# Kernel optimization log

Hardware: AMD Instinct MI355X
Metric: run time of the kernel (lower is better)

Reference implementation:

```python
import jax, jax.numpy as jnp
import numpy as np

H, C = 4, 64            # heads, channels per head (graph_hidden_channels)
GHC = H * C             # concat width = 256
FIN = 32                # num_node_features
NHID = 256
NOUT = 256
NEG_SLOPE = 0.2         # PyG GATConv default negative_slope


def gat_conv(x, src, dst, n, W, a_src, a_dst, bias):
    # x: [N, Fin], W: [Fin, H*C], a_src/a_dst: [H, C], bias: [H*C]
    h = (x @ W).reshape(n, H, C)                       # [N,H,C]
    s = (h * a_src).sum(-1)                            # [N,H] src logits
    d = (h * a_dst).sum(-1)                            # [N,H] dst logits
    e = jax.nn.leaky_relu(s[src] + d[dst], NEG_SLOPE)  # [E,H]
    m = jax.ops.segment_max(e, dst, num_segments=n)    # segment softmax (stable)
    ex = jnp.exp(e - m[dst])
    denom = jax.ops.segment_sum(ex, dst, num_segments=n)
    alpha = ex / jnp.maximum(denom[dst], 1e-16)        # [E,H]
    msg = h[src] * alpha[:, :, None]                   # [E,H,C]
    out = jax.ops.segment_sum(msg, dst, num_segments=n)
    return out.reshape(n, GHC) + bias


def setup_inputs() -> dict:
    key = jax.random.key(0)
    ks = jax.random.split(key, 32)
    N, E, G = 50000, 800000, 256
    inp = {
        'x': jax.random.normal(ks[0], (N, FIN), dtype=jnp.float32),
        'edge_index': jax.random.randint(ks[1], (2, E), 0, N, dtype=jnp.int32),
        'batch': jnp.sort(jax.random.randint(ks[2], (N,), 0, G, dtype=jnp.int32)),
        'num_graphs': G,
    }
    def p(k, shape):
        return jax.random.normal(k, shape, dtype=jnp.float32) * 0.05
    # three GATConv layers + head linears
    ins = [FIN, C, C]
    i = 3
    for l, fin in enumerate(ins, start=1):
        inp[f'W{l}'] = p(ks[i], (fin, GHC)); i += 1
        inp[f'a{l}s'] = p(ks[i], (H, C)); i += 1
        inp[f'a{l}d'] = p(ks[i], (H, C)); i += 1
        inp[f'b{l}'] = p(ks[i], (GHC,)); i += 1
        inp[f'hl{l}_w'] = p(ks[i], (GHC, C)); i += 1
        inp[f'hl{l}_b'] = p(ks[i], (C,)); i += 1
    inp['mh1_w'] = p(ks[i], (C, NHID)); i += 1
    inp['mh1_b'] = p(ks[i], (NHID,)); i += 1
    inp['mh2_w'] = p(ks[i], (NHID, NOUT)); i += 1
    inp['mh2_b'] = p(ks[i], (NOUT,))
    return inp


def reference(x, edge_index, batch, num_graphs,
              W1, a1s, a1d, b1, hl1_w, hl1_b,
              W2, a2s, a2d, b2, hl2_w, hl2_b,
              W3, a3s, a3d, b3, hl3_w, hl3_b,
              mh1_w, mh1_b, mh2_w, mh2_b):
    n = x.shape[0]
    loops = jnp.arange(n, dtype=edge_index.dtype)  # PyG add_self_loops=True
    src = jnp.concatenate([edge_index[0], loops])
    dst = jnp.concatenate([edge_index[1], loops])

    h = gat_conv(x, src, dst, n, W1, a1s, a1d, b1)
    h = jax.nn.relu(h @ hl1_w + hl1_b)
    h = gat_conv(h, src, dst, n, W2, a2s, a2d, b2)
    h = jax.nn.relu(h @ hl2_w + hl2_b)
    h = gat_conv(h, src, dst, n, W3, a3s, a3d, b3)
    h = h @ hl3_w + hl3_b                      # no relu before pooling (as in source)

    sums = jax.ops.segment_sum(h, batch, num_segments=num_graphs)
    cnt = jax.ops.segment_sum(jnp.ones((n,), h.dtype), batch, num_segments=num_graphs)
    g = sums / jnp.maximum(cnt, 1.0)[:, None]  # global_mean_pool

    g = jax.nn.relu(g @ mh1_w + mh1_b)
    return g @ mh2_w + mh2_b
```

## Files before the change

kernel.cpp:

```cpp
#include <hip/hip_runtime.h>
#include <hip/hip_bf16.h>
#include <hip/hip_fp16.h>
#include <math.h>

#define HD 4
#define CH 64
#define GHC 256
#define NEG 0.2f
#define CHUNK 4096
#define BCAP 16384

#define WAVE_SYNC() do { __builtin_amdgcn_wave_barrier(); \
                         asm volatile("s_waitcnt lgkmcnt(0)" ::: "memory"); } while (0)

typedef _Float16 f16x8 __attribute__((ext_vector_type(8)));
typedef float f32x4 __attribute__((ext_vector_type(4)));

__device__ __forceinline__ float wsum32(float v){
  #pragma unroll
  for (int o = 16; o > 0; o >>= 1) v += __shfl_xor(v, o);
  return v;
}

__global__ __launch_bounds__(256)
void front_kernel(const int* __restrict__ ei, int E, int N, int cb_blocks,
                  int* __restrict__ bres, unsigned* __restrict__ pairs,
                  const float* __restrict__ W1, const float* __restrict__ a1s,
                  const float* __restrict__ a1d, const float* __restrict__ b1,
                  const float* __restrict__ h1w, const float* __restrict__ h1b,
                  const float* __restrict__ W2, const float* __restrict__ a2s,
                  const float* __restrict__ a2d, const float* __restrict__ b2,
                  const float* __restrict__ h2w, const float* __restrict__ h2b,
                  const float* __restrict__ W3, const float* __restrict__ a3s,
                  const float* __restrict__ a3d, const float* __restrict__ b3,
                  const float* __restrict__ h3w, const float* __restrict__ h3b,
                  __half* __restrict__ Wpk1, float* __restrict__ Psd1, float* __restrict__ cb1,
                  __half* __restrict__ Wpk2, __half* __restrict__ Ppk2, float* __restrict__ cb2,
                  float* __restrict__ Wcp3, __half* __restrict__ Ppk3, float* __restrict__ cb3,
                  const int* __restrict__ batch, int G, int* __restrict__ bnd)
{
  __shared__ unsigned staged[CHUNK];
  __shared__ unsigned short bkt[CHUNK];
  __shared__ int cnts[256], loff[256], gpos[256];
  const int t = threadIdx.x;

  if (blockIdx.x < cb_blocks){
    const int tot = E + N;
    const int cbase = blockIdx.x * CHUNK;
    if (cbase >= tot) return;

    cnts[t] = 0;
    __syncthreads();

    unsigned myp[CHUNK / 256];
    int myb[CHUNK / 256], myr[CHUNK / 256];
    #pragma unroll
    for (int j = 0; j < CHUNK / 256; j++){
      int i = cbase + t + j * 256;
      myb[j] = -1;
      if (i < tot){
        int src, dst;
        if (i < E){ src = ei[i]; dst = ei[E + i]; }
        else { src = dst = i - E; }
        myb[j] = dst >> 8;
        myp[j] = (unsigned)src | ((unsigned)dst << 16);
        myr[j] = atomicAdd(&cnts[myb[j]], 1);
      }
    }
    __syncthreads();

    int v = cnts[t];
    loff[t] = v;
    __syncthreads();
    for (int o = 1; o < 256; o <<= 1){
      int tv = (t >= o) ? loff[t - o] : 0;
      __syncthreads();
      loff[t] += tv;
      __syncthreads();
    }
    int excl = loff[t] - v;
    __syncthreads();
    loff[t] = excl;
    __syncthreads();

    #pragma unroll
    for (int j = 0; j < CHUNK / 256; j++){
      if (myb[j] >= 0){
        int slot = loff[myb[j]] + myr[j];
        staged[slot] = myp[j];
        bkt[slot] = (unsigned short)myb[j];
      }
    }
    if (v > 0) gpos[t] = atomicAdd(&bres[t], v);
    __syncthreads();

    int total = min(CHUNK, tot - cbase);
    for (int i = t; i < total; i += 256){
      int b = bkt[i];
      int addr = b * BCAP + gpos[b] + (i - loff[b]);
      pairs[addr] = staged[i];
    }
    return;
  }

  const int blk = blockIdx.x - cb_blocks;
  if (blk >= 163){
    int g = (blk - 163) * 256 + t;
    if (g > G) return;
    if (g == G){ bnd[G] = N; return; }
    int lo = 0, hi = N;
    while (lo < hi){ int mid = (lo + hi) >> 1; if (batch[mid] < g) lo = mid + 1; else hi = mid; }
    bnd[g] = lo;
    return;
  }
  const float *W, *as, *ad, *bl, *hlw, *hlb;
  float *cb;
  int FIN, b, layer;
  if (blk < 33){
    W = W1; as = a1s; ad = a1d; bl = b1; hlw = h1w; hlb = h1b;
    cb = cb1; FIN = 32; b = blk; layer = 1;
  } else if (blk < 98){
    W = W2; as = a2s; ad = a2d; bl = b2; hlw = h2w; hlb = h2b;
    cb = cb2; FIN = 64; b = blk - 33; layer = 2;
  } else {
    W = W3; as = a3s; ad = a3d; bl = b3; hlw = h3w; hlb = h3b;
    cb = cb3; FIN = 64; b = blk - 98; layer = 3;
  }
  if (b < FIN){
    const int c = t >> 2, h = t & 3;
    const float* wrow = W + b * GHC + h * 64;
    float acc = 0.f;
    #pragma unroll 8
    for (int j = 0; j < 64; j++)
      acc += wrow[j] * hlw[(h * 64 + j) * CH + c];
    const int k = h * FIN + b;
    if (layer == 3){
      Wcp3[k * CH + c] = acc;
    } else {
      int ks = k >> 5, nt = c >> 4;
      int lane = (((k & 31) >> 3) << 4) | (c & 15);
      int idx = ((ks * 4 + nt) * 64 + lane) * 8 + (k & 7);
      __half* Wpk = (layer == 1) ? Wpk1 : Wpk2;
      Wpk[idx] = __float2half(acc);
    }
    if (t < 8){
      const int hh = t & 3;
      const float* a = (t < 4) ? as : ad;
      const float* wr2 = W + b * GHC + hh * 64;
      float p = 0.f;
      #pragma unroll 8
      for (int j = 0; j < 64; j++) p += wr2[j] * a[hh * 64 + j];
      if (layer == 1){
        Psd1[b * 8 + t] = p;
      } else {
        int kk = b;
        int ks = kk >> 5;
        int lane = (((kk & 31) >> 3) << 4) | t;
        int idx = (ks * 64 + lane) * 8 + (kk & 7);
        __half* Ppk = (layer == 2) ? Ppk2 : Ppk3;
        Ppk[idx] = __float2half(p);
      }
    }
  } else if (t < CH){
    float acc = hlb[t];
    for (int j = 0; j < GHC; j++) acc += bl[j] * hlw[j * CH + t];
    cb[t] = acc;
  }
}

__global__ __launch_bounds__(256)
void mid_kernel(const unsigned* __restrict__ pairs, const int* __restrict__ bres,
                int N, int Etot, int nbuck,
                int* __restrict__ offs, unsigned short* __restrict__ csr,
                const float* __restrict__ x, const float* __restrict__ Psd,
                float* __restrict__ s_log, float* __restrict__ d_log,
                __half* __restrict__ xh0)
{
  __shared__ int dcnt[256], doff[256], bscan[256];
  const int t = threadIdx.x;

  if (blockIdx.x < nbuck){
    const int b = blockIdx.x;
    int bv = bres[t];
    bscan[t] = bv;
    __syncthreads();
    for (int o = 1; o < 256; o <<= 1){
      int tv = (t >= o) ? bscan[t - o] : 0;
      __syncthreads();
      bscan[t] += tv;
      __syncthreads();
    }
    const int beg = bscan[b] - bres[b];
    const int cnt = bres[b];
    const unsigned* pb = pairs + (size_t)b * BCAP;
    dcnt[t] = 0;
    __syncthreads();
    for (int i = t; i < cnt; i += 256)
      atomicAdd(&dcnt[(pb[i] >> 16) & 255], 1);
    __syncthreads();
    int v = dcnt[t];
    doff[t] = v;
    __syncthreads();
    for (int o = 1; o < 256; o <<= 1){
      int tv = (t >= o) ? doff[t - o] : 0;
      __syncthreads();
      doff[t] += tv;
      __syncthreads();
    }
    int excl = doff[t] - v;
    __syncthreads();
    doff[t] = excl;
    __syncthreads();
    int node = (b << 8) + t;
    if (node < N) offs[node] = beg + doff[t];
    if (b == 0 && t == 0) offs[N] = Etot;
    dcnt[t] = 0;
    __syncthreads();
    for (int i = t; i < cnt; i += 256){
      unsigned pr = pb[i];
      int l = (pr >> 16) & 255;
      int pos = beg + doff[l] + atomicAdd(&dcnt[l], 1);
      csr[pos] = (unsigned short)(pr & 0xFFFF);
    }
    return;
  }

  int idx = (blockIdx.x - nbuck) * 256 + t;
  int node = idx >> 3, q = idx & 7;
  if (node >= N) return;
  const float* xr = x + (size_t)node * 32;
  float v = 0.f;
  #pragma unroll 8
  for (int k = 0; k < 32; k++) v += xr[k] * Psd[k * 8 + q];
  if (q < 4){
    s_log[node * 4 + q] = v;
    __half2 h0 = __floats2half2_rn(xr[q*8+0], xr[q*8+1]);
    __half2 h1 = __floats2half2_rn(xr[q*8+2], xr[q*8+3]);
    __half2 h2 = __floats2half2_rn(xr[q*8+4], xr[q*8+5]);
    __half2 h3 = __floats2half2_rn(xr[q*8+6], xr[q*8+7]);
    uint4 u;
    u.x = *reinterpret_cast<const unsigned*>(&h0);
    u.y = *reinterpret_cast<const unsigned*>(&h1);
    u.z = *reinterpret_cast<const unsigned*>(&h2);
    u.w = *reinterpret_cast<const unsigned*>(&h3);
    *reinterpret_cast<uint4*>(xh0 + (size_t)node * 32 + q * 8) = u;
  } else {
    d_log[node * 4 + (q - 4)] = v;
  }
}

template<int F, int ZW>
__global__ __launch_bounds__(512)
void gat_layer_fused(const __half* __restrict__ xin, const float* __restrict__ s_in,
                     const float* __restrict__ d_in_, const int* __restrict__ off,
                     const unsigned short* __restrict__ csr,
                     const __half* __restrict__ Wpk, const float* __restrict__ cb,
                     const __half* __restrict__ Ppk,
                     __half* __restrict__ xo, float* __restrict__ s_out,
                     float* __restrict__ d_out_, int N)
{
  constexpr int ZP = ZW + 8;
  __shared__ float4 qa[8][2][32];
  __shared__ int    qs[8][2][32];
  __shared__ __half z_lds[16][ZP];
  __shared__ float  outs[16][68];
  __shared__ float  cbs[64];
  const int tid  = threadIdx.x;
  const int wv   = tid >> 6;
  const int lane = tid & 63;
  const int half = lane >> 5;
  const int l32  = lane & 31;
  const int n0 = blockIdx.x * 16;
  const int n = n0 + wv * 2 + half;
  const bool valid = n < N;
  if (tid < 64) cbs[tid] = cb[tid];

  int beg = 0, deg = 0;
  if (valid){ beg = off[n]; deg = off[n + 1] - beg; }

  float d4[4] = {0.f, 0.f, 0.f, 0.f};
  if (valid){
    float4 d4v = reinterpret_cast<const float4*>(d_in_)[n];
    d4[0] = d4v.x; d4[1] = d4v.y; d4[2] = d4v.z; d4[3] = d4v.w;
  }

  float den[4], ex[4];
  int s = 0;
  {
    const bool act = valid && (l32 < deg);
    if (act){
      s = csr[beg + l32];
      float4 sl = reinterpret_cast<const float4*>(s_in)[s];
      float t[4] = {sl.x, sl.y, sl.z, sl.w};
      #pragma unroll
      for (int i = 0; i < 4; i++){
        float u = t[i] + d4[i]; u = (u >= 0.f) ? u : NEG * u;
        ex[i] = __expf(u);
      }
    } else {
      #pragma unroll
      for (int i = 0; i < 4; i++) ex[i] = 0.f;
    }
    #pragma unroll
    for (int i = 0; i < 4; i++) den[i] = wsum32(ex[i]);
  }
  for (int base = 32; base < deg; base += 32){
    const int k = base + l32;
    float e2[4] = {0.f, 0.f, 0.f, 0.f};
    if (k < deg){
      int s2 = csr[beg + k];
      float4 sl = reinterpret_cast<const float4*>(s_in)[s2];
      float t[4] = {sl.x, sl.y, sl.z, sl.w};
      #pragma unroll
      for (int i = 0; i < 4; i++){
        float u = t[i] + d4[i]; u = (u >= 0.f) ? u : NEG * u;
        e2[i] = __expf(u);
      }
    }
    #pragma unroll
    for (int i = 0; i < 4; i++) den[i] += wsum32(e2[i]);
  }

  float dninv[4];
  #pragma unroll
  for (int i = 0; i < 4; i++) dninv[i] = 1.f / fmaxf(den[i], 1e-16f);

  float a0[4] = {0.f,0.f,0.f,0.f};
  float a1[4] = {0.f,0.f,0.f,0.f};
  const float4* qap = qa[wv][half];
  const int*    qsp = qs[wv][half];

  auto accum = [&](int cnt){
    int cntR = (cnt + 3) & ~3;
    if (F == 64){
      const __half* xb = xin + 2 * l32;
      for (int e0 = 0; e0 < cntR; e0 += 4){
        float4 al[4]; int sv[4]; unsigned uv[4];
        #pragma unroll
        for (int j = 0; j < 4; j++){ al[j] = qap[e0 + j]; sv[j] = qsp[e0 + j]; }
        #pragma unroll
        for (int j = 0; j < 4; j++)
          uv[j] = *reinterpret_cast<const unsigned*>(xb + sv[j] * 64);
        #pragma unroll
        for (int j = 0; j < 4; j++){
          float2 f = __half22float2(*reinterpret_cast<const __half2*>(&uv[j]));
          a0[0] += al[j].x * f.x; a1[0] += al[j].x * f.y;
          a0[1] += al[j].y * f.x; a1[1] += al[j].y * f.y;
          a0[2] += al[j].z * f.x; a1[2] += al[j].z * f.y;
          a0[3] += al[j].w * f.x; a1[3] += al[j].w * f.y;
        }
      }
    } else {
      const __half* xb = xin + l32;
      for (int e0 = 0; e0 < cntR; e0 += 4){
        float4 al[4]; int sv[4]; __half hv[4];
        #pragma unroll
        for (int j = 0; j < 4; j++){ al[j] = qap[e0 + j]; sv[j] = qsp[e0 + j]; }
        #pragma unroll
        for (int j = 0; j < 4; j++)
          hv[j] = xb[sv[j] * 32];
        #pragma unroll
        for (int j = 0; j < 4; j++){
          float xv = __half2float(hv[j]);
          a0[0] += al[j].x * xv;
          a0[1] += al[j].y * xv;
          a0[2] += al[j].z * xv;
          a0[3] += al[j].w * xv;
        }
      }
    }
  };

  if (deg <= 32){
    qa[wv][half][l32] = make_float4(ex[0] * dninv[0], ex[1] * dninv[1],
                                    ex[2] * dninv[2], ex[3] * dninv[3]);
    qs[wv][half][l32] = s;
    WAVE_SYNC();
    accum(deg);
  } else {
    for (int base = 0; base < deg; base += 32){
      const int k = base + l32;
      int s2 = 0; float al[4] = {0.f, 0.f, 0.f, 0.f};
      if (k < deg){
        s2 = csr[beg + k];
        float4 sl = reinterpret_cast<const float4*>(s_in)[s2];
        float t[4] = {sl.x, sl.y, sl.z, sl.w};
        #pragma unroll
        for (int i = 0; i < 4; i++){
          float u = t[i] + d4[i]; u = (u >= 0.f) ? u : NEG * u;
          al[i] = __expf(u) * dninv[i];
        }
      }
      qa[wv][half][l32] = make_float4(al[0], al[1], al[2], al[3]);
      qs[wv][half][l32] = s2;
      WAVE_SYNC();
      accum(min(32, deg - base));
      WAVE_SYNC();
    }
  }

  {
    const int r = wv * 2 + half;
    if (F == 64){
      #pragma unroll
      for (int h = 0; h < 4; h++){
        __half2 hv = __floats2half2_rn(a0[h], a1[h]);
        *reinterpret_cast<unsigned*>(&z_lds[r][h * 64 + 2 * l32]) =
            *reinterpret_cast<const unsigned*>(&hv);
      }
    } else {
      #pragma unroll
      for (int h = 0; h < 4; h++)
        z_lds[r][h * 32 + l32] = __float2half(a0[h]);
    }
  }
  __syncthreads();

  const int row = lane & 15, kg = lane >> 4;
  if (wv < 4){
    const int nt = wv;
    f32x4 acc = {0.f,0.f,0.f,0.f};
    const f16x8* wp = reinterpret_cast<const f16x8*>(Wpk) + lane;
    #pragma unroll
    for (int ks = 0; ks < ZW / 32; ks++){
      f16x8 af = *reinterpret_cast<const f16x8*>(&z_lds[row][kg * 8 + ks * 32]);
      acc = __builtin_amdgcn_mfma_f32_16x16x32_f16(af, wp[(ks*4+nt)*64], acc, 0,0,0);
    }
    #pragma unroll
    for (int r = 0; r < 4; r++){
      int rr = kg * 4 + r;
      outs[rr][nt * 16 + row] = fmaxf(acc[r] + cbs[nt * 16 + row], 0.f);
    }
  }
  __syncthreads();

  if (tid < 256){
    int nn = tid >> 4, part = tid & 15;
    int node = n0 + nn;
    if (node < N){
      const float* o = &outs[nn][part * 4];
      __half2 h0 = __floats2half2_rn(o[0], o[1]);
      __half2 h1 = __floats2half2_rn(o[2], o[3]);
      uint2 u;
      u.x = *reinterpret_cast<const unsigned*>(&h0);
      u.y = *reinterpret_cast<const unsigned*>(&h1);
      *reinterpret_cast<uint2*>(xo + (size_t)node * 64 + part * 4) = u;
    }
  }

  if (wv == 4){
    f32x4 lacc = {0.f,0.f,0.f,0.f};
    const f16x8* pp = reinterpret_cast<const f16x8*>(Ppk) + lane;
    #pragma unroll
    for (int ks = 0; ks < 2; ks++){
      f16x8 af;
      #pragma unroll
      for (int j = 0; j < 8; j++) af[j] = (_Float16)outs[row][ks * 32 + kg * 8 + j];
      lacc = __builtin_amdgcn_mfma_f32_16x16x32_f16(af, pp[ks * 64], lacc, 0,0,0);
    }
    if (row < 8){
      float* dst = (row < 4) ? s_out : d_out_;
      int q = row & 3;
      #pragma unroll
      for (int r = 0; r < 4; r++){
        int node = n0 + kg * 4 + r;
        if (node < N) dst[node * 4 + q] = lacc[r];
      }
    }
  }
}

template<int F>
__global__ __launch_bounds__(256)
void gat_aggregate_z(const __half* __restrict__ xin, const float* __restrict__ s_log,
                     const float* __restrict__ d_log, const int* __restrict__ off,
                     const unsigned short* __restrict__ csr, __half* __restrict__ z, int N)
{
  __shared__ float4 qa[4][2][32];
  __shared__ int    qs[4][2][32];
  const int wv   = threadIdx.x >> 6;
  const int lane = threadIdx.x & 63;
  const int half = lane >> 5;
  const int l32  = lane & 31;
  const int n = blockIdx.x * 8 + wv * 2 + half;
  const bool valid = n < N;

  int beg = 0, deg = 0;
  if (valid){ beg = off[n]; deg = off[n + 1] - beg; }

  float d4[4] = {0.f, 0.f, 0.f, 0.f};
  if (valid){
    float4 d4v = reinterpret_cast<const float4*>(d_log)[n];
    d4[0] = d4v.x; d4[1] = d4v.y; d4[2] = d4v.z; d4[3] = d4v.w;
  }

  float den[4], ex[4];
  int s = 0;
  {
    const bool act = valid && (l32 < deg);
    if (act){
      s = csr[beg + l32];
      float4 sl = reinterpret_cast<const float4*>(s_log)[s];
      float t[4] = {sl.x, sl.y, sl.z, sl.w};
      #pragma unroll
      for (int i = 0; i < 4; i++){
        float u = t[i] + d4[i]; u = (u >= 0.f) ? u : NEG * u;
        ex[i] = __expf(u);
      }
    } else {
      #pragma unroll
      for (int i = 0; i < 4; i++) ex[i] = 0.f;
    }
    #pragma unroll
    for (int i = 0; i < 4; i++) den[i] = wsum32(ex[i]);
  }
  for (int base = 32; base < deg; base += 32){
    const int k = base + l32;
    float e2[4] = {0.f, 0.f, 0.f, 0.f};
    if (k < deg){
      int s2 = csr[beg + k];
      float4 sl = reinterpret_cast<const float4*>(s_log)[s2];
      float t[4] = {sl.x, sl.y, sl.z, sl.w};
      #pragma unroll
      for (int i = 0; i < 4; i++){
        float u = t[i] + d4[i]; u = (u >= 0.f) ? u : NEG * u;
        e2[i] = __expf(u);
      }
    }
    #pragma unroll
    for (int i = 0; i < 4; i++) den[i] += wsum32(e2[i]);
  }

  float dninv[4];
  #pragma unroll
  for (int i = 0; i < 4; i++) dninv[i] = 1.f / fmaxf(den[i], 1e-16f);

  float a0[4] = {0.f,0.f,0.f,0.f};
  float a1[4] = {0.f,0.f,0.f,0.f};
  const float4* qap = qa[wv][half];
  const int*    qsp = qs[wv][half];

  auto accum = [&](int cnt){
    int cntR = (cnt + 3) & ~3;
    const __half* xb = xin + 2 * l32;
    for (int e0 = 0; e0 < cntR; e0 += 4){
      float4 al[4]; int sv[4]; unsigned uv[4];
      #pragma unroll
      for (int j = 0; j < 4; j++){ al[j] = qap[e0 + j]; sv[j] = qsp[e0 + j]; }
      #pragma unroll
      for (int j = 0; j < 4; j++)
        uv[j] = *reinterpret_cast<const unsigned*>(xb + sv[j] * 64);
      #pragma unroll
      for (int j = 0; j < 4; j++){
        float2 f = __half22float2(*reinterpret_cast<const __half2*>(&uv[j]));
        a0[0] += al[j].x * f.x; a1[0] += al[j].x * f.y;
        a0[1] += al[j].y * f.x; a1[1] += al[j].y * f.y;
        a0[2] += al[j].z * f.x; a1[2] += al[j].z * f.y;
        a0[3] += al[j].w * f.x; a1[3] += al[j].w * f.y;
      }
    }
  };

  if (deg <= 32){
    qa[wv][half][l32] = make_float4(ex[0] * dninv[0], ex[1] * dninv[1],
                                    ex[2] * dninv[2], ex[3] * dninv[3]);
    qs[wv][half][l32] = s;
    WAVE_SYNC();
    accum(deg);
  } else {
    for (int base = 0; base < deg; base += 32){
      const int k = base + l32;
      int s2 = 0; float al[4] = {0.f, 0.f, 0.f, 0.f};
      if (k < deg){
        s2 = csr[beg + k];
        float4 sl = reinterpret_cast<const float4*>(s_log)[s2];
        float t[4] = {sl.x, sl.y, sl.z, sl.w};
        #pragma unroll
        for (int i = 0; i < 4; i++){
          float u = t[i] + d4[i]; u = (u >= 0.f) ? u : NEG * u;
          al[i] = __expf(u) * dninv[i];
        }
      }
      qa[wv][half][l32] = make_float4(al[0], al[1], al[2], al[3]);
      qs[wv][half][l32] = s2;
      WAVE_SYNC();
      accum(min(32, deg - base));
      WAVE_SYNC();
    }
  }

  if (valid){
    const size_t zb = (size_t)n * 256 + 2 * l32;
    #pragma unroll
    for (int h = 0; h < 4; h++){
      __half2 hv = __floats2half2_rn(a0[h], a1[h]);
      *reinterpret_cast<unsigned*>(z + zb + h * 64) =
          *reinterpret_cast<const unsigned*>(&hv);
    }
  }
}

__global__ __launch_bounds__(256)
void pool_partial(const __half* __restrict__ z3, const int* __restrict__ bnd,
                  float* __restrict__ psum)
{
  const int blk = blockIdx.x, tid = threadIdx.x;
  const int g = blk >> 2, part = blk & 3;
  const int s = bnd[g], e = bnd[g + 1];
  const int cp = tid & 127, rp = tid >> 7;
  float ax = 0.f, ay = 0.f;
  for (int n = s + part + 4 * rp; n < e; n += 8){
    __half2 hv = *reinterpret_cast<const __half2*>(z3 + (size_t)n * 256 + 2 * cp);
    float2 f = __half22float2(hv);
    ax += f.x; ay += f.y;
  }
  __shared__ float shx[2][128], shy[2][128];
  shx[rp][cp] = ax; shy[rp][cp] = ay;
  __syncthreads();
  if (tid < 128){
    psum[(size_t)blk * 256 + 2 * tid]     = shx[0][tid] + shx[1][tid];
    psum[(size_t)blk * 256 + 2 * tid + 1] = shy[0][tid] + shy[1][tid];
  }
}

__global__ __launch_bounds__(256)
void head_mlp(const float* __restrict__ psum, const int* __restrict__ bnd,
              const float* __restrict__ Wcp3, const float* __restrict__ cb3,
              const float* __restrict__ m1w, const float* __restrict__ m1b,
              const float* __restrict__ m2w, const float* __restrict__ m2b,
              float* __restrict__ out)
{
  const int g = blockIdx.x, tid = threadIdx.x;
  const float cnt = (float)max(bnd[g + 1] - bnd[g], 1);
  __shared__ float zbar[256];
  const float* pb = psum + (size_t)g * 1024;
  zbar[tid] = (pb[tid] + pb[256 + tid] + pb[512 + tid] + pb[768 + tid]) / cnt;
  __syncthreads();
  const int c = tid & 63, part = tid >> 6;
  float tp = 0.f;
  #pragma unroll 8
  for (int k = part * 64; k < part * 64 + 64; k++) tp += zbar[k] * Wcp3[k * 64 + c];
  __shared__ float tsh[4][64];
  tsh[part][c] = tp;
  __syncthreads();
  __shared__ float tvec[64];
  if (tid < 64)
    tvec[tid] = tsh[0][tid] + tsh[1][tid] + tsh[2][tid] + tsh[3][tid] + cb3[tid];
  __syncthreads();
  float a = m1b[tid];
  #pragma unroll 8
  for (int cc = 0; cc < 64; cc++) a += tvec[cc] * m1w[cc * 256 + tid];
  __shared__ float g1row[256];
  g1row[tid] = fmaxf(a, 0.f);
  __syncthreads();
  float o = m2b[tid];
  #pragma unroll 8
  for (int k = 0; k < 256; k++) o += g1row[k] * m2w[k * 256 + tid];
  out[g * 256 + tid] = o;
}

extern "C" void kernel_launch(void* const* d_in, const int* in_sizes, int n_in,
                              void* d_out, int out_size, void* d_ws, size_t ws_size,
                              hipStream_t stream)
{
  const float* x     = (const float*)d_in[0];
  const int*   ei    = (const int*)d_in[1];
  const int*   batch = (const int*)d_in[2];
  const float* W1  = (const float*)d_in[4];
  const float* a1s = (const float*)d_in[5];
  const float* a1d = (const float*)d_in[6];
  const float* b1  = (const float*)d_in[7];
  const float* h1w = (const float*)d_in[8];
  const float* h1b = (const float*)d_in[9];
  const float* W2  = (const float*)d_in[10];
  const float* a2s = (const float*)d_in[11];
  const float* a2d = (const float*)d_in[12];
  const float* b2  = (const float*)d_in[13];
  const float* h2w = (const float*)d_in[14];
  const float* h2b = (const float*)d_in[15];
  const float* W3  = (const float*)d_in[16];
  const float* a3s = (const float*)d_in[17];
  const float* a3d = (const float*)d_in[18];
  const float* b3  = (const float*)d_in[19];
  const float* h3w = (const float*)d_in[20];
  const float* h3b = (const float*)d_in[21];
  const float* m1w = (const float*)d_in[22];
  const float* m1b = (const float*)d_in[23];
  const float* m2w = (const float*)d_in[24];
  const float* m2b = (const float*)d_in[25];

  const int N = in_sizes[0] / 32;
  const int E = in_sizes[1] / 2;
  const int G = out_size / 256;
  const int Etot = E + N;
  const int nbuck = (N + 255) >> 8;

  char* p = (char*)d_ws;
  auto alloc = [&](size_t bytes) -> void* {
    void* r = (void*)p;
    p += ((bytes + 255) / 256) * 256;
    return r;
  };
  __half* zbuf   = (__half*)alloc((size_t)N * GHC * 2);
  __half* xh0    = (__half*)alloc((size_t)N * 32 * 2);
  __half* xh1    = (__half*)alloc((size_t)N * CH * 2);
  __half* xh2    = (__half*)alloc((size_t)N * CH * 2);
  float* s_logA  = (float*)alloc((size_t)N * HD * 4);
  float* d_logA  = (float*)alloc((size_t)N * HD * 4);
  float* s_logB  = (float*)alloc((size_t)N * HD * 4);
  float* d_logB  = (float*)alloc((size_t)N * HD * 4);
  int*   offs    = (int*)alloc((size_t)(N + 1) * 4);
  unsigned short* csr = (unsigned short*)alloc((size_t)Etot * 2);
  unsigned* pairs = (unsigned*)alloc((size_t)nbuck * BCAP * 4);
  int*    bres   = (int*)alloc(256 * 4);
  __half* Ppk2   = (__half*)alloc(1024 * 2);
  __half* Ppk3   = (__half*)alloc(1024 * 2);
  int*   bnd     = (int*)alloc((size_t)(G + 1) * 4);
  float* psum    = (float*)alloc((size_t)G * 4 * 256 * 4);
  float* Wcp3    = (float*)alloc(256 * 64 * 4);
  float* Psd1    = (float*)alloc(32 * 8 * 4);
  float* cb1     = (float*)alloc(64 * 4);
  float* cb2     = (float*)alloc(64 * 4);
  float* cb3     = (float*)alloc(64 * 4);
  __half* Wpk1   = (__half*)alloc(128 * 64 * 2);
  __half* Wpk2   = (__half*)alloc(256 * 64 * 2);

  hipMemsetAsync(bres, 0, 5120, stream);

  const int cb_blocks = (Etot + CHUNK - 1) / CHUNK;
  const int fuse_blocks = 163 + (G + 256) / 256;
  front_kernel<<<cb_blocks + fuse_blocks, 256, 0, stream>>>(
      ei, E, N, cb_blocks, bres, pairs,
      W1, a1s, a1d, b1, h1w, h1b,
      W2, a2s, a2d, b2, h2w, h2b,
      W3, a3s, a3d, b3, h3w, h3b,
      Wpk1, Psd1, cb1, Wpk2, Ppk2, cb2, Wcp3, Ppk3, cb3,
      batch, G, bnd);

  const int lg_blocks = ((size_t)N * 8 + 255) / 256;
  mid_kernel<<<nbuck + lg_blocks, 256, 0, stream>>>(
      pairs, bres, N, Etot, nbuck, offs, csr,
      x, Psd1, s_logA, d_logA, xh0);

  const int fgrid = (N + 15) / 16;
  gat_layer_fused<32, 128><<<fgrid, 512, 0, stream>>>(xh0, s_logA, d_logA, offs, csr,
                                                      Wpk1, cb1, Ppk2, xh1, s_logB, d_logB, N);
  gat_layer_fused<64, 256><<<fgrid, 512, 0, stream>>>(xh1, s_logB, d_logB, offs, csr,
                                                      Wpk2, cb2, Ppk3, xh2, s_logA, d_logA, N);

  const int ab = (N + 7) / 8;
  gat_aggregate_z<64><<<ab, 256, 0, stream>>>(xh2, s_logA, d_logA, offs, csr, zbuf, N);

  pool_partial<<<G * 4, 256, 0, stream>>>(zbuf, bnd, psum);
  head_mlp<<<G, 256, 0, stream>>>(psum, bnd, Wcp3, cb3, m1w, m1b, m2w, m2b, (float*)d_out);
}
```

Baseline: 150.1 us.

## Fuse layer-3 head linear into fused GAT kernel and pool 64-wide outputs

Replaces the separate layer-3 aggregate kernel, which wrote a 256-wide fp16 z buffer per node, with the fused GAT layer template (no ReLU, no logits), which applies the folded W3·hl3 projection via MFMA and writes 64-wide node outputs. Pooling then reads 64 channels instead of 256, and the head MLP no longer applies the Wcp3 projection after pooling. This cuts the large z write and read traffic. The cost is a per-node projection in place of a per-graph one, and fp16 rounding now falls at a different point.

```diff
diff --git a/kernel.cpp b/kernel.cpp
--- a/kernel.cpp
+++ b/kernel.cpp
@@ -36,7 +36,7 @@
                   const float* __restrict__ h3w, const float* __restrict__ h3b,
                   __half* __restrict__ Wpk1, float* __restrict__ Psd1, float* __restrict__ cb1,
                   __half* __restrict__ Wpk2, __half* __restrict__ Ppk2, float* __restrict__ cb2,
-                  float* __restrict__ Wcp3, __half* __restrict__ Ppk3, float* __restrict__ cb3,
+                  __half* __restrict__ Wpk3, __half* __restrict__ Ppk3, float* __restrict__ cb3,
                   const int* __restrict__ batch, int G, int* __restrict__ bnd)
 {
   __shared__ unsigned staged[CHUNK];
@@ -134,13 +134,11 @@
     for (int j = 0; j < 64; j++)
       acc += wrow[j] * hlw[(h * 64 + j) * CH + c];
     const int k = h * FIN + b;
-    if (layer == 3){
-      Wcp3[k * CH + c] = acc;
-    } else {
+    {
       int ks = k >> 5, nt = c >> 4;
       int lane = (((k & 31) >> 3) << 4) | (c & 15);
       int idx = ((ks * 4 + nt) * 64 + lane) * 8 + (k & 7);
-      __half* Wpk = (layer == 1) ? Wpk1 : Wpk2;
+      __half* Wpk = (layer == 1) ? Wpk1 : ((layer == 2) ? Wpk2 : Wpk3);
       Wpk[idx] = __float2half(acc);
     }
     if (t < 8){
@@ -249,7 +247,7 @@
   }
 }
 
-template<int F, int ZW>
+template<int F, int ZW, bool RELU, bool LOGITS>
 __global__ __launch_bounds__(512)
 void gat_layer_fused(const __half* __restrict__ xin, const float* __restrict__ s_in,
                      const float* __restrict__ d_in_, const int* __restrict__ off,
@@ -429,7 +427,9 @@
     #pragma unroll
     for (int r = 0; r < 4; r++){
       int rr = kg * 4 + r;
-      outs[rr][nt * 16 + row] = fmaxf(acc[r] + cbs[nt * 16 + row], 0.f);
+      float v = acc[r] + cbs[nt * 16 + row];
+      if (RELU) v = fmaxf(v, 0.f);
+      outs[rr][nt * 16 + row] = v;
     }
   }
   __syncthreads();
@@ -448,7 +448,7 @@
     }
   }
 
-  if (wv == 4){
+  if (LOGITS && wv == 4){
     f32x4 lacc = {0.f,0.f,0.f,0.f};
     const f16x8* pp = reinterpret_cast<const f16x8*>(Ppk) + lane;
     #pragma unroll
@@ -470,182 +470,44 @@
   }
 }
 
-template<int F>
 __global__ __launch_bounds__(256)
-void gat_aggregate_z(const __half* __restrict__ xin, const float* __restrict__ s_log,
-                     const float* __restrict__ d_log, const int* __restrict__ off,
-                     const unsigned short* __restrict__ csr, __half* __restrict__ z, int N)
-{
-  __shared__ float4 qa[4][2][32];
-  __shared__ int    qs[4][2][32];
-  const int wv   = threadIdx.x >> 6;
-  const int lane = threadIdx.x & 63;
-  const int half = lane >> 5;
-  const int l32  = lane & 31;
-  const int n = blockIdx.x * 8 + wv * 2 + half;
-  const bool valid = n < N;
-
-  int beg = 0, deg = 0;
-  if (valid){ beg = off[n]; deg = off[n + 1] - beg; }
-
-  float d4[4] = {0.f, 0.f, 0.f, 0.f};
-  if (valid){
-    float4 d4v = reinterpret_cast<const float4*>(d_log)[n];
-    d4[0] = d4v.x; d4[1] = d4v.y; d4[2] = d4v.z; d4[3] = d4v.w;
-  }
-
-  float den[4], ex[4];
-  int s = 0;
-  {
-    const bool act = valid && (l32 < deg);
-    if (act){
-      s = csr[beg + l32];
-      float4 sl = reinterpret_cast<const float4*>(s_log)[s];
-      float t[4] = {sl.x, sl.y, sl.z, sl.w};
-      #pragma unroll
-      for (int i = 0; i < 4; i++){
-        float u = t[i] + d4[i]; u = (u >= 0.f) ? u : NEG * u;
-        ex[i] = __expf(u);
-      }
-    } else {
-      #pragma unroll
-      for (int i = 0; i < 4; i++) ex[i] = 0.f;
-    }
-    #pragma unroll
-    for (int i = 0; i < 4; i++) den[i] = wsum32(ex[i]);
-  }
-  for (int base = 32; base < deg; base += 32){
-    const int k = base + l32;
-    float e2[4] = {0.f, 0.f, 0.f, 0.f};
-    if (k < deg){
-      int s2 = csr[beg + k];
-      float4 sl = reinterpret_cast<const float4*>(s_log)[s2];
-      float t[4] = {sl.x, sl.y, sl.z, sl.w};
-      #pragma unroll
-      for (int i = 0; i < 4; i++){
-        float u = t[i] + d4[i]; u = (u >= 0.f) ? u : NEG * u;
-        e2[i] = __expf(u);
-      }
-    }
-    #pragma unroll
-    for (int i = 0; i < 4; i++) den[i] += wsum32(e2[i]);
-  }
-
-  float dninv[4];
-  #pragma unroll
-  for (int i = 0; i < 4; i++) dninv[i] = 1.f / fmaxf(den[i], 1e-16f);
-
-  float a0[4] = {0.f,0.f,0.f,0.f};
-  float a1[4] = {0.f,0.f,0.f,0.f};
-  const float4* qap = qa[wv][half];
-  const int*    qsp = qs[wv][half];
-
-  auto accum = [&](int cnt){
-    int cntR = (cnt + 3) & ~3;
-    const __half* xb = xin + 2 * l32;
-    for (int e0 = 0; e0 < cntR; e0 += 4){
-      float4 al[4]; int sv[4]; unsigned uv[4];
-      #pragma unroll
-      for (int j = 0; j < 4; j++){ al[j] = qap[e0 + j]; sv[j] = qsp[e0 + j]; }
-      #pragma unroll
-      for (int j = 0; j < 4; j++)
-        uv[j] = *reinterpret_cast<const unsigned*>(xb + sv[j] * 64);
-      #pragma unroll
-      for (int j = 0; j < 4; j++){
-        float2 f = __half22float2(*reinterpret_cast<const __half2*>(&uv[j]));
-        a0[0] += al[j].x * f.x; a1[0] += al[j].x * f.y;
-        a0[1] += al[j].y * f.x; a1[1] += al[j].y * f.y;
-        a0[2] += al[j].z * f.x; a1[2] += al[j].z * f.y;
-        a0[3] += al[j].w * f.x; a1[3] += al[j].w * f.y;
-      }
-    }
-  };
-
-  if (deg <= 32){
-    qa[wv][half][l32] = make_float4(ex[0] * dninv[0], ex[1] * dninv[1],
-                                    ex[2] * dninv[2], ex[3] * dninv[3]);
-    qs[wv][half][l32] = s;
-    WAVE_SYNC();
-    accum(deg);
-  } else {
-    for (int base = 0; base < deg; base += 32){
-      const int k = base + l32;
-      int s2 = 0; float al[4] = {0.f, 0.f, 0.f, 0.f};
-      if (k < deg){
-        s2 = csr[beg + k];
-        float4 sl = reinterpret_cast<const float4*>(s_log)[s2];
-        float t[4] = {sl.x, sl.y, sl.z, sl.w};
-        #pragma unroll
-        for (int i = 0; i < 4; i++){
-          float u = t[i] + d4[i]; u = (u >= 0.f) ? u : NEG * u;
-          al[i] = __expf(u) * dninv[i];
-        }
-      }
-      qa[wv][half][l32] = make_float4(al[0], al[1], al[2], al[3]);
-      qs[wv][half][l32] = s2;
-      WAVE_SYNC();
-      accum(min(32, deg - base));
-      WAVE_SYNC();
-    }
-  }
-
-  if (valid){
-    const size_t zb = (size_t)n * 256 + 2 * l32;
-    #pragma unroll
-    for (int h = 0; h < 4; h++){
-      __half2 hv = __floats2half2_rn(a0[h], a1[h]);
-      *reinterpret_cast<unsigned*>(z + zb + h * 64) =
-          *reinterpret_cast<const unsigned*>(&hv);
-    }
-  }
-}
-
-__global__ __launch_bounds__(256)
-void pool_partial(const __half* __restrict__ z3, const int* __restrict__ bnd,
+void pool_partial(const __half* __restrict__ x3, const int* __restrict__ bnd,
                   float* __restrict__ psum)
 {
   const int blk = blockIdx.x, tid = threadIdx.x;
   const int g = blk >> 2, part = blk & 3;
   const int s = bnd[g], e = bnd[g + 1];
-  const int cp = tid & 127, rp = tid >> 7;
+  const int cp = tid & 31, rp = tid >> 5;
   float ax = 0.f, ay = 0.f;
-  for (int n = s + part + 4 * rp; n < e; n += 8){
-    __half2 hv = *reinterpret_cast<const __half2*>(z3 + (size_t)n * 256 + 2 * cp);
+  for (int n = s + part + 4 * rp; n < e; n += 32){
+    __half2 hv = *reinterpret_cast<const __half2*>(x3 + (size_t)n * 64 + 2 * cp);
     float2 f = __half22float2(hv);
     ax += f.x; ay += f.y;
   }
-  __shared__ float shx[2][128], shy[2][128];
+  __shared__ float shx[8][32], shy[8][32];
   shx[rp][cp] = ax; shy[rp][cp] = ay;
   __syncthreads();
-  if (tid < 128){
-    psum[(size_t)blk * 256 + 2 * tid]     = shx[0][tid] + shx[1][tid];
-    psum[(size_t)blk * 256 + 2 * tid + 1] = shy[0][tid] + shy[1][tid];
+  if (tid < 32){
+    float sx = 0.f, sy = 0.f;
+    #pragma unroll
+    for (int r = 0; r < 8; r++){ sx += shx[r][tid]; sy += shy[r][tid]; }
+    psum[(size_t)blk * 64 + 2 * tid]     = sx;
+    psum[(size_t)blk * 64 + 2 * tid + 1] = sy;
   }
 }
 
 __global__ __launch_bounds__(256)
 void head_mlp(const float* __restrict__ psum, const int* __restrict__ bnd,
-              const float* __restrict__ Wcp3, const float* __restrict__ cb3,
               const float* __restrict__ m1w, const float* __restrict__ m1b,
               const float* __restrict__ m2w, const float* __restrict__ m2b,
               float* __restrict__ out)
 {
   const int g = blockIdx.x, tid = threadIdx.x;
   const float cnt = (float)max(bnd[g + 1] - bnd[g], 1);
-  __shared__ float zbar[256];
-  const float* pb = psum + (size_t)g * 1024;
-  zbar[tid] = (pb[tid] + pb[256 + tid] + pb[512 + tid] + pb[768 + tid]) / cnt;
-  __syncthreads();
-  const int c = tid & 63, part = tid >> 6;
-  float tp = 0.f;
-  #pragma unroll 8
-  for (int k = part * 64; k < part * 64 + 64; k++) tp += zbar[k] * Wcp3[k * 64 + c];
-  __shared__ float tsh[4][64];
-  tsh[part][c] = tp;
-  __syncthreads();
   __shared__ float tvec[64];
+  const float* pb = psum + (size_t)g * 256;
   if (tid < 64)
-    tvec[tid] = tsh[0][tid] + tsh[1][tid] + tsh[2][tid] + tsh[3][tid] + cb3[tid];
+    tvec[tid] = (pb[tid] + pb[64 + tid] + pb[128 + tid] + pb[192 + tid]) / cnt;
   __syncthreads();
   float a = m1b[tid];
   #pragma unroll 8
@@ -701,10 +563,10 @@
     p += ((bytes + 255) / 256) * 256;
     return r;
   };
-  __half* zbuf   = (__half*)alloc((size_t)N * GHC * 2);
   __half* xh0    = (__half*)alloc((size_t)N * 32 * 2);
   __half* xh1    = (__half*)alloc((size_t)N * CH * 2);
   __half* xh2    = (__half*)alloc((size_t)N * CH * 2);
+  __half* xh3    = (__half*)alloc((size_t)N * CH * 2);
   float* s_logA  = (float*)alloc((size_t)N * HD * 4);
   float* d_logA  = (float*)alloc((size_t)N * HD * 4);
   float* s_logB  = (float*)alloc((size_t)N * HD * 4);
@@ -716,14 +578,14 @@
   __half* Ppk2   = (__half*)alloc(1024 * 2);
   __half* Ppk3   = (__half*)alloc(1024 * 2);
   int*   bnd     = (int*)alloc((size_t)(G + 1) * 4);
-  float* psum    = (float*)alloc((size_t)G * 4 * 256 * 4);
-  float* Wcp3    = (float*)alloc(256 * 64 * 4);
+  float* psum    = (float*)alloc((size_t)G * 4 * 64 * 4);
   float* Psd1    = (float*)alloc(32 * 8 * 4);
   float* cb1     = (float*)alloc(64 * 4);
   float* cb2     = (float*)alloc(64 * 4);
   float* cb3     = (float*)alloc(64 * 4);
   __half* Wpk1   = (__half*)alloc(128 * 64 * 2);
   __half* Wpk2   = (__half*)alloc(256 * 64 * 2);
+  __half* Wpk3   = (__half*)alloc(256 * 64 * 2);
 
   hipMemsetAsync(bres, 0, 5120, stream);
 
@@ -734,7 +596,7 @@
       W1, a1s, a1d, b1, h1w, h1b,
       W2, a2s, a2d, b2, h2w, h2b,
       W3, a3s, a3d, b3, h3w, h3b,
-      Wpk1, Psd1, cb1, Wpk2, Ppk2, cb2, Wcp3, Ppk3, cb3,
+      Wpk1, Psd1, cb1, Wpk2, Ppk2, cb2, Wpk3, Ppk3, cb3,
       batch, G, bnd);
 
   const int lg_blocks = ((size_t)N * 8 + 255) / 256;
@@ -743,14 +605,13 @@
       x, Psd1, s_logA, d_logA, xh0);
 
   const int fgrid = (N + 15) / 16;
-  gat_layer_fused<32, 128><<<fgrid, 512, 0, stream>>>(xh0, s_logA, d_logA, offs, csr,
-                                                      Wpk1, cb1, Ppk2, xh1, s_logB, d_logB, N);
-  gat_layer_fused<64, 256><<<fgrid, 512, 0, stream>>>(xh1, s_logB, d_logB, offs, csr,
-                                                      Wpk2, cb2, Ppk3, xh2, s_logA, d_logA, N);
-
-  const int ab = (N + 7) / 8;
-  gat_aggregate_z<64><<<ab, 256, 0, stream>>>(xh2, s_logA, d_logA, offs, csr, zbuf, N);
-
-  pool_partial<<<G * 4, 256, 0, stream>>>(zbuf, bnd, psum);
-  head_mlp<<<G, 256, 0, stream>>>(psum, bnd, Wcp3, cb3, m1w, m1b, m2w, m2b, (float*)d_out);
+  gat_layer_fused<32, 128, true,  true ><<<fgrid, 512, 0, stream>>>(
+      xh0, s_logA, d_logA, offs, csr, Wpk1, cb1, Ppk2, xh1, s_logB, d_logB, N);
+  gat_layer_fused<64, 256, true,  true ><<<fgrid, 512, 0, stream>>>(
+      xh1, s_logB, d_logB, offs, csr, Wpk2, cb2, Ppk3, xh2, s_logA, d_logA, N);
+  gat_layer_fused<64, 256, false, false><<<fgrid, 512, 0, stream>>>(
+      xh2, s_logA, d_logA, offs, csr, Wpk3, cb3, nullptr, xh3, nullptr, nullptr, N);
+
+  pool_partial<<<G * 4, 256, 0, stream>>>(xh3, bnd, psum);
+  head_mlp<<<G, 256, 0, stream>>>(psum, bnd, m1w, m1b, m2w, m2b, (float*)d_out);
 }
```

New measurement: 152.4 us. Within noise of the previous version (+1.5%).
